# Kernel tuning notes

Measured on AMD Instinct MI355X. Metric: run time of the kernel, lower is better.

Reference implementation:

```python
import jax, jax.numpy as jnp
import numpy as np

N = 100000   # nodes
E = 1000000  # edges
F_IN = 15    # node feature dim
H = 64       # hidden dim
EMB = 128    # embedding dim
R = 13       # relations
NB = 4       # bases


def _xavier(key, shape):
    fan_in, fan_out = shape[-2], shape[-1]
    lim = float(np.sqrt(6.0 / (fan_in + fan_out)))
    return jax.random.uniform(key, shape, jnp.float32, -lim, lim)


def setup_inputs() -> dict:
    key = jax.random.key(0)
    ks = jax.random.split(key, 24)
    inp = {}
    inp["node_features"] = jax.random.normal(ks[0], (N, F_IN), jnp.float32)
    inp["edge_index"] = jax.random.randint(ks[1], (2, E), 0, N, jnp.int32)
    inp["edge_type"] = jax.random.randint(ks[2], (E,), 0, R, jnp.int32)
    # input projection (15 -> 64)
    inp["W_in"] = _xavier(ks[3], (F_IN, H)); inp["b_in"] = jnp.zeros((H,), jnp.float32)
    # RGCN layer 0
    inp["Wself0"] = _xavier(ks[4], (H, H)); inp["bself0"] = jnp.zeros((H,), jnp.float32)
    inp["bases0"] = _xavier(ks[5], (NB, H, H))
    inp["coeffs0"] = _xavier(ks[6], (R, NB))
    # RGCN layer 1
    inp["Wself1"] = _xavier(ks[7], (H, H)); inp["bself1"] = jnp.zeros((H,), jnp.float32)
    inp["bases1"] = _xavier(ks[8], (NB, H, H))
    inp["coeffs1"] = _xavier(ks[9], (R, NB))
    # readout MLP (2H -> H -> EMB)
    inp["Wr1"] = _xavier(ks[10], (2 * H, H)); inp["br1"] = jnp.zeros((H,), jnp.float32)
    inp["Wr2"] = _xavier(ks[11], (H, EMB)); inp["br2"] = jnp.zeros((EMB,), jnp.float32)
    # node projection (H -> EMB)
    inp["Wnp"] = _xavier(ks[12], (H, EMB)); inp["bnp"] = jnp.zeros((EMB,), jnp.float32)
    return inp


def _rgcn_layer(h, src, tgt, etype, Wself, bself, bases, coeffs):
    # h: (N, H). Sum over relations of per-relation gather+matmul+scatter-add
    # == single scatter over all edges with per-edge relation weight.
    # Basis decomposition: W_r = sum_b coeffs[r,b] * bases[b].
    h_src = h[src]                 # (E, H) gather
    c_e = coeffs[etype]            # (E, NB) per-edge basis coefficients
    msg = jnp.zeros((h_src.shape[0], bases.shape[2]), h.dtype)
    for b in range(bases.shape[0]):  # fixed small loop over NB=4 bases
        msg = msg + c_e[:, b:b + 1] * (h_src @ bases[b])
    agg = jax.ops.segment_sum(msg, tgt, num_segments=h.shape[0])  # (N, H)
    # NOTE: original code computes degree norm but never applies it (dead code),
    # so aggregation is an unnormalized scatter-add, reproduced faithfully here.
    return jax.nn.relu(h @ Wself + bself + agg)  # dropout is identity in eval


def reference(node_features, edge_index, edge_type, W_in, b_in,
              Wself0, bself0, bases0, coeffs0,
              Wself1, bself1, bases1, coeffs1,
              Wr1, br1, Wr2, br2, Wnp, bnp):
    src, tgt = edge_index[0], edge_index[1]
    h = node_features @ W_in + b_in                      # (N, H)
    h = _rgcn_layer(h, src, tgt, edge_type, Wself0, bself0, bases0, coeffs0)
    h = _rgcn_layer(h, src, tgt, edge_type, Wself1, bself1, bases1, coeffs1)
    # graph readout: mean + max pooling over nodes -> MLP
    g = jnp.concatenate([h.mean(axis=0), h.max(axis=0)])  # (2H,)
    graph_emb = jax.nn.relu(g @ Wr1 + br1) @ Wr2 + br2    # (EMB,)
    node_emb = h @ Wnp + bnp                              # (N, EMB)
    return graph_emb, node_emb
```

## Files before the change

kernel.cpp:

```cpp
#include <hip/hip_runtime.h>
#include <hip/hip_bf16.h>

#define NN 100000
#define EE 1000000
#define FIN 15
#define HH 64
#define EMBD 128
#define RR 13
#define NBASE 4
#define NP 391

typedef __hip_bfloat16 bf16;
typedef __attribute__((ext_vector_type(8))) short short8;
typedef __attribute__((ext_vector_type(4))) float f32x4;

__device__ __forceinline__ float b2f(bf16 x) { return __bfloat162float(x); }
__device__ __forceinline__ float bcast(float v, int l) {
    return __uint_as_float(__builtin_amdgcn_readlane(__float_as_uint(v), l));
}
__device__ __forceinline__ int bcasti(int v, int l) {
    return (int)__builtin_amdgcn_readlane((unsigned)v, l);
}
__device__ __forceinline__ unsigned short f2bu(float f) {
    bf16 t = __float2bfloat16(f);
    return *reinterpret_cast<unsigned short*>(&t);
}
__device__ __forceinline__ float bu2f(unsigned u) {
    return __uint_as_float(u << 16);
}

__global__ void k_detect(const void* __restrict__ win, int* __restrict__ flag) {
    int tid = threadIdx.x;
    const bf16* p = (const bf16*)win;
    int cnt = 0;
    for (int i = tid; i < FIN * HH; i += 64) {
        float v = b2f(p[i]);
        if (!(fabsf(v) < 0.3f)) cnt++;
    }
#pragma unroll
    for (int off = 32; off > 0; off >>= 1) cnt += __shfl_down(cnt, off, 64);
    if (tid == 0) *flag = (cnt > 40) ? 1 : 0;
}

struct ConvTab {
    const void* in[17];
    int n[17];
    int cum[18];
};

__global__ void k_convert_all(ConvTab tab, float* __restrict__ base,
                              const int* __restrict__ flag) {
    int g = blockIdx.x * 256 + threadIdx.x;
    if (g >= tab.cum[17]) return;
    int t = 0;
#pragma unroll
    for (int i = 0; i < 17; ++i) if (g >= tab.cum[i + 1]) t = i + 1;
    int local = g - tab.cum[t];
    if (local >= tab.n[t]) return;
    float v;
    if (*flag) v = ((const float*)tab.in[t])[local];
    else       v = b2f(((const bf16*)tab.in[t])[local]);
    base[g] = v;
}

__global__ void k_zero(int* __restrict__ a, int n) {
    int i = blockIdx.x * 256 + threadIdx.x;
    if (i < n) a[i] = 0;
}

__global__ void k_hist(const int* __restrict__ tgt, int* __restrict__ count,
                       int* __restrict__ rank) {
    int e = blockIdx.x * 256 + threadIdx.x;
    if (e >= EE) return;
    rank[e] = atomicAdd(&count[tgt[e]], 1);
}

__global__ void k_scan1(const int* __restrict__ count, int* __restrict__ scanned,
                        int* __restrict__ partials) {
    __shared__ int buf[256];
    int tid = threadIdx.x;
    int i = blockIdx.x * 256 + tid;
    int v = (i < NN) ? count[i] : 0;
    buf[tid] = v;
    __syncthreads();
    for (int off = 1; off < 256; off <<= 1) {
        int t = (tid >= off) ? buf[tid - off] : 0;
        __syncthreads();
        buf[tid] += t;
        __syncthreads();
    }
    if (i < NN) scanned[i] = buf[tid] - v;
    if (tid == 255) partials[blockIdx.x] = buf[255];
}

__global__ void k_scan2(int* __restrict__ partials) {
    __shared__ int buf[512];
    int tid = threadIdx.x;
    int v = (tid < NP) ? partials[tid] : 0;
    buf[tid] = v;
    __syncthreads();
    for (int off = 1; off < 512; off <<= 1) {
        int t = (tid >= off) ? buf[tid - off] : 0;
        __syncthreads();
        buf[tid] += t;
        __syncthreads();
    }
    if (tid < NP) partials[tid] = buf[tid] - v;
}

__global__ void k_scatter(const int* __restrict__ src, const int* __restrict__ tgt,
                          const int* __restrict__ et, const int* __restrict__ rank,
                          const int* __restrict__ scanned, const int* __restrict__ partials,
                          int* __restrict__ packed) {
    int e = blockIdx.x * 256 + threadIdx.x;
    if (e >= EE) return;
    int t = tgt[e];
    int pos = scanned[t] + partials[t >> 8] + rank[e];
    packed[pos] = src[e] | (et[e] << 17);
}

__global__ void k_wcat(const float* __restrict__ bases0, const float* __restrict__ Wself0,
                       const float* __restrict__ bases1, const float* __restrict__ Wself1,
                       unsigned short* __restrict__ W0, unsigned short* __restrict__ W1) {
    int idx = blockIdx.x * 256 + threadIdx.x;
    if (idx >= HH * 320) return;
    int n = idx / 320, k = idx - n * 320;
    int b = k >> 6, kk = k & 63;
    float v0 = (b < 4) ? bases0[b * 4096 + kk * 64 + n] : Wself0[kk * 64 + n];
    float v1 = (b < 4) ? bases1[b * 4096 + kk * 64 + n] : Wself1[kk * 64 + n];
    W0[idx] = f2bu(v0);
    W1[idx] = f2bu(v1);
}


__global__ void k_input_proj(const float* __restrict__ nf, const float* __restrict__ Win,
                             const float* __restrict__ bin, unsigned short* __restrict__ h) {
    __shared__ float w[FIN * HH];
    __shared__ float bb[HH];
    int tid = threadIdx.x;
    for (int i = tid; i < FIN * HH; i += 256) w[i] = Win[i];
    if (tid < HH) bb[tid] = bin[tid];
    __syncthreads();
    int idx = blockIdx.x * 256 + tid;
    if (idx >= NN * HH) return;
    int n = idx >> 6, j = idx & 63;
    float acc = bb[j];
    const float* row = nf + n * FIN;
#pragma unroll
    for (int k = 0; k < FIN; ++k) acc = fmaf(row[k], w[k * HH + j], acc);
    h[idx] = f2bu(acc);
}

__global__ void __launch_bounds__(256, 4)
k_layer(const unsigned short* __restrict__ hin, const int* __restrict__ packed,
        const int* __restrict__ count, const int* __restrict__ scanned,
        const int* __restrict__ partials, const float* __restrict__ coeffs,
        const unsigned short* __restrict__ Wc, const float* __restrict__ bself,
        unsigned short* __restrict__ hout) {
    __shared__ __align__(16) unsigned short Sb[16 * 264];
    int tid = threadIdx.x;
    int lane = tid & 63;
    int wv = tid >> 6;
    int t0 = blockIdx.x * 16;

    float S[4][NBASE];
#pragma unroll
    for (int ln = 0; ln < 4; ++ln)
        S[ln][0] = S[ln][1] = S[ln][2] = S[ln][3] = 0.f;

#pragma unroll
    for (int ln = 0; ln < 4; ++ln) {
        int t = t0 + wv * 4 + ln;
        int cnt = count[t];
        int s0 = scanned[t] + partials[t >> 8];
        for (int base = 0; base < cnt; base += 64) {
            int pk = 0;
            if (base + lane < cnt) pk = packed[s0 + base + lane];
            int m = min(64, cnt - base);
            for (int j = 0; j < m; j += 8) {
                float hv[8];
                float4 cv[8];
#pragma unroll
                for (int k = 0; k < 8; ++k) {
                    int v = bcasti(pk, j + k);
                    int s = v & 0x1FFFF;
                    int r = (v >> 17) & 0xF;
                    hv[k] = bu2f((unsigned)hin[s * HH + lane]);
                    cv[k] = *(const float4*)(coeffs + r * NBASE);
                }
#pragma unroll
                for (int k = 0; k < 8; ++k) {
                    float hk = ((j + k) < m) ? hv[k] : 0.f;
                    S[ln][0] = fmaf(cv[k].x, hk, S[ln][0]);
                    S[ln][1] = fmaf(cv[k].y, hk, S[ln][1]);
                    S[ln][2] = fmaf(cv[k].z, hk, S[ln][2]);
                    S[ln][3] = fmaf(cv[k].w, hk, S[ln][3]);
                }
            }
        }
    }
#pragma unroll
    for (int ln = 0; ln < 4; ++ln)
#pragma unroll
        for (int b = 0; b < NBASE; ++b)
            Sb[(wv * 4 + ln) * 264 + b * 64 + lane] = f2bu(S[ln][b]);
    __syncthreads();

    int m16 = lane & 15;
    int g = lane >> 4;
    f32x4 acc = {0.f, 0.f, 0.f, 0.f};
    const unsigned short* brow = Wc + (wv * 16 + m16) * 320 + g * 8;
#pragma unroll
    for (int kb = 0; kb < 8; ++kb) {
        short8 a = *(const short8*)(&Sb[m16 * 264 + kb * 32 + g * 8]);
        short8 b = *(const short8*)(brow + kb * 32);
        acc = __builtin_amdgcn_mfma_f32_16x16x32_bf16(a, b, acc, 0, 0, 0);
    }
    const unsigned short* hrow = hin + (t0 + m16) * HH + g * 8;
#pragma unroll
    for (int kb = 0; kb < 2; ++kb) {
        short8 a = *(const short8*)(hrow + kb * 32);
        short8 b = *(const short8*)(brow + 256 + kb * 32);
        acc = __builtin_amdgcn_mfma_f32_16x16x32_bf16(a, b, acc, 0, 0, 0);
    }
    int col = wv * 16 + m16;
    float bias = bself[col];
#pragma unroll
    for (int r = 0; r < 4; ++r) {
        int row = g * 4 + r;
        hout[(t0 + row) * HH + col] = f2bu(fmaxf(acc[r] + bias, 0.f));
    }
}

__global__ void k_reduce(const unsigned short* __restrict__ h, float* __restrict__ psum,
                         float* __restrict__ pmax) {
    __shared__ float ls[256], lm[256];
    int tid = threadIdx.x;
    int j = tid & 63;
    int slot = tid >> 6;
    float s = 0.f, m = -1e30f;
    for (int n = blockIdx.x * 4 + slot; n < NN; n += gridDim.x * 4) {
        float v = bu2f((unsigned)h[n * HH + j]);
        s += v;
        m = fmaxf(m, v);
    }
    ls[tid] = s; lm[tid] = m;
    __syncthreads();
    if (tid < 64) {
        s = ls[tid] + ls[tid + 64] + ls[tid + 128] + ls[tid + 192];
        m = fmaxf(fmaxf(lm[tid], lm[tid + 64]), fmaxf(lm[tid + 128], lm[tid + 192]));
        psum[blockIdx.x * 64 + tid] = s;
        pmax[blockIdx.x * 64 + tid] = m;
    }
}

__global__ void k_finish(const float* __restrict__ psum, const float* __restrict__ pmax,
                         const float* __restrict__ Wr1, const float* __restrict__ br1,
                         const float* __restrict__ Wr2, const float* __restrict__ br2,
                         void* __restrict__ out, const int* __restrict__ flag) {
    __shared__ float ls[256], lm[256];
    __shared__ float g[2 * HH];
    __shared__ float tbuf[HH];
    int tid = threadIdx.x;
    int j = tid & 63;
    int slot = tid >> 6;
    float s = 0.f, m = -1e30f;
    for (int i = slot; i < 256; i += 4) {
        s += psum[i * 64 + j];
        m = fmaxf(m, pmax[i * 64 + j]);
    }
    ls[tid] = s; lm[tid] = m;
    __syncthreads();
    if (tid < 64) {
        s = ls[tid] + ls[tid + 64] + ls[tid + 128] + ls[tid + 192];
        m = fmaxf(fmaxf(lm[tid], lm[tid + 64]), fmaxf(lm[tid + 128], lm[tid + 192]));
        g[tid] = s * (1.0f / NN);
        g[64 + tid] = m;
    }
    __syncthreads();
    if (tid < 64) {
        float acc = br1[tid];
#pragma unroll 8
        for (int k = 0; k < 2 * HH; ++k) acc = fmaf(g[k], Wr1[k * HH + tid], acc);
        tbuf[tid] = fmaxf(acc, 0.f);
    }
    __syncthreads();
    if (tid < EMBD) {
        float acc = br2[tid];
#pragma unroll 8
        for (int k = 0; k < HH; ++k) acc = fmaf(tbuf[k], Wr2[k * EMBD + tid], acc);
        if (*flag) ((float*)out)[tid] = acc;
        else       ((bf16*)out)[tid] = __float2bfloat16(acc);
    }
}

__global__ void k_node_emb2(const unsigned short* __restrict__ h, const float* __restrict__ Wnp,
                            const float* __restrict__ bnp, void* __restrict__ out,
                            const int* __restrict__ flag) {
    int tid = threadIdx.x;
    int lane = tid & 63;
    int wv = tid >> 6;
    int n0 = blockIdx.x * 32 + wv * 8;
    float hval[8];
#pragma unroll
    for (int ln = 0; ln < 8; ++ln)
        hval[ln] = bu2f((unsigned)h[(n0 + ln) * HH + lane]);
    float b0 = bnp[lane], b1 = bnp[64 + lane];
    float acc0[8], acc1[8];
#pragma unroll
    for (int ln = 0; ln < 8; ++ln) { acc0[ln] = b0; acc1[ln] = b1; }
#pragma unroll 8
    for (int k = 0; k < HH; ++k) {
        float w0 = Wnp[k * EMBD + lane];
        float w1 = Wnp[k * EMBD + 64 + lane];
#pragma unroll
        for (int ln = 0; ln < 8; ++ln) {
            float hv = bcast(hval[ln], k);
            acc0[ln] = fmaf(hv, w0, acc0[ln]);
            acc1[ln] = fmaf(hv, w1, acc1[ln]);
        }
    }
    if (*flag) {
        float* o = (float*)out + EMBD;
#pragma unroll
        for (int ln = 0; ln < 8; ++ln) {
            o[(long)(n0 + ln) * EMBD + lane] = acc0[ln];
            o[(long)(n0 + ln) * EMBD + 64 + lane] = acc1[ln];
        }
    } else {
        bf16* o = (bf16*)out + EMBD;
#pragma unroll
        for (int ln = 0; ln < 8; ++ln) {
            o[(long)(n0 + ln) * EMBD + lane] = __float2bfloat16(acc0[ln]);
            o[(long)(n0 + ln) * EMBD + 64 + lane] = __float2bfloat16(acc1[ln]);
        }
    }
}

extern "C" void kernel_launch(void* const* d_in, const int* in_sizes, int n_in,
                              void* d_out, int out_size, void* d_ws, size_t ws_size,
                              hipStream_t stream) {
    const int* eidx  = (const int*)d_in[1];
    const int* etype = (const int*)d_in[2];
    const int* src = eidx;
    const int* tgt = eidx + EE;

    int* flag = (int*)d_ws;
    float* base = (float*)d_ws + 16;

    const int fidx[17] = {0, 3, 4, 5, 6, 7, 8, 9, 10, 11, 12, 13, 14, 15, 16, 17, 18};
    ConvTab tab;
    float* conv[19];
    int cum = 0;
    for (int t = 0; t < 17; ++t) {
        int i = fidx[t];
        tab.in[t] = d_in[i];
        tab.n[t] = in_sizes[i];
        tab.cum[t] = cum;
        conv[i] = base + cum;
        cum += (in_sizes[i] + 15) & ~15;
    }
    tab.cum[17] = cum;

    k_detect<<<1, 64, 0, stream>>>(d_in[3], flag);
    k_convert_all<<<(cum + 255) / 256, 256, 0, stream>>>(tab, base, flag);

    float* p = base + cum;
    float* psum = p;  p += 256 * 64;
    float* pmax = p;  p += 256 * 64;
    int* count    = (int*)p;           p += NN;
    int* scanned  = (int*)p;           p += NN;
    int* partials = (int*)p;           p += 512;
    int* rank     = (int*)p;           p += EE;
    int* packed   = (int*)p;           p += EE;
    unsigned short* hbf0 = (unsigned short*)p;
    unsigned short* hbf1 = hbf0 + (size_t)NN * HH;
    unsigned short* Wc0  = hbf1 + (size_t)NN * HH;
    unsigned short* Wc1  = Wc0 + HH * 320;

    const float* nf      = conv[0];
    const float* Win     = conv[3];
    const float* bin     = conv[4];
    const float* Wself0  = conv[5];
    const float* bself0  = conv[6];
    const float* bases0  = conv[7];
    const float* coeffs0 = conv[8];
    const float* Wself1  = conv[9];
    const float* bself1  = conv[10];
    const float* bases1  = conv[11];
    const float* coeffs1 = conv[12];
    const float* Wr1     = conv[13];
    const float* br1     = conv[14];
    const float* Wr2     = conv[15];
    const float* br2     = conv[16];
    const float* Wnp     = conv[17];
    const float* bnp     = conv[18];

    const int NHB = (NN * HH) / 256;
    const int SMB = NN / 32;
    const int LYB = NN / 16;
    const int EB  = (EE + 255) / 256;

    k_zero<<<(NN + 255) / 256, 256, 0, stream>>>(count, NN);
    k_hist<<<EB, 256, 0, stream>>>(tgt, count, rank);
    k_scan1<<<NP, 256, 0, stream>>>(count, scanned, partials);
    k_scan2<<<1, 512, 0, stream>>>(partials);
    k_scatter<<<EB, 256, 0, stream>>>(src, tgt, etype, rank, scanned, partials, packed);

    k_wcat<<<(HH * 320 + 255) / 256, 256, 0, stream>>>(bases0, Wself0, bases1, Wself1, Wc0, Wc1);
    k_input_proj<<<NHB, 256, 0, stream>>>(nf, Win, bin, hbf0);

    k_layer<<<LYB, 256, 0, stream>>>(hbf0, packed, count, scanned, partials, coeffs0, Wc0, bself0, hbf1);
    k_layer<<<LYB, 256, 0, stream>>>(hbf1, packed, count, scanned, partials, coeffs1, Wc1, bself1, hbf0);

    k_reduce<<<256, 256, 0, stream>>>(hbf0, psum, pmax);
    k_finish<<<1, 256, 0, stream>>>(psum, pmax, Wr1, br1, Wr2, br2, d_out, flag);
    k_node_emb2<<<SMB, 256, 0, stream>>>(hbf0, Wnp, bnp, d_out, flag);
}
```

Baseline: 434.7 us.

## Pad per-node edge lists with sentinels and move node projection onto MFMA

Each node's CSR segment is padded to a multiple of 8 and filled with a sentinel relation whose coefficients are zero. This removes per-edge bounds masking in the layer gather, which now processes edges in groups of 16 or 8 and raises occupancy to 6 blocks per SM. The node-embedding projection is rewritten to use bf16 MFMA with a hi/lo split of Wnp to keep fp32-like accuracy. The cost is extra fill and prep kernels plus a larger packed buffer. The sentinel path relies on the padded coefficient table and on the source index 0 reads being harmless.

```diff
diff --git a/kernel.cpp b/kernel.cpp
--- a/kernel.cpp
+++ b/kernel.cpp
@@ -9,6 +9,8 @@
 #define RR 13
 #define NBASE 4
 #define NP 391
+#define CAP 1700128
+#define SENT (15 << 17)
 
 typedef __hip_bfloat16 bf16;
 typedef __attribute__((ext_vector_type(8))) short short8;
@@ -68,6 +70,11 @@
     if (i < n) a[i] = 0;
 }
 
+__global__ void k_fill(int* __restrict__ a, int n, int val) {
+    int i = blockIdx.x * 256 + threadIdx.x;
+    if (i < n) a[i] = val;
+}
+
 __global__ void k_hist(const int* __restrict__ tgt, int* __restrict__ count,
                        int* __restrict__ rank) {
     int e = blockIdx.x * 256 + threadIdx.x;
@@ -80,7 +87,7 @@
     __shared__ int buf[256];
     int tid = threadIdx.x;
     int i = blockIdx.x * 256 + tid;
-    int v = (i < NN) ? count[i] : 0;
+    int v = (i < NN) ? ((count[i] + 7) & ~7) : 0;
     buf[tid] = v;
     __syncthreads();
     for (int off = 1; off < 256; off <<= 1) {
@@ -117,6 +124,14 @@
     int t = tgt[e];
     int pos = scanned[t] + partials[t >> 8] + rank[e];
     packed[pos] = src[e] | (et[e] << 17);
+}
+
+__global__ void k_coef(const float* __restrict__ c0, const float* __restrict__ c1,
+                       float* __restrict__ o0, float* __restrict__ o1) {
+    int t = threadIdx.x;
+    int r = t >> 2, b = t & 3;
+    o0[t] = (r < RR) ? c0[r * NBASE + b] : 0.f;
+    o1[t] = (r < RR) ? c1[r * NBASE + b] : 0.f;
 }
 
 __global__ void k_wcat(const float* __restrict__ bases0, const float* __restrict__ Wself0,
@@ -132,6 +147,16 @@
     W1[idx] = f2bu(v1);
 }
 
+__global__ void k_wt(const float* __restrict__ Wnp, unsigned short* __restrict__ WT) {
+    int idx = blockIdx.x * 256 + threadIdx.x;
+    if (idx >= EMBD * HH) return;
+    int c = idx >> 6, k = idx & 63;
+    float w = Wnp[k * EMBD + c];
+    unsigned short hi = f2bu(w);
+    WT[idx] = hi;
+    WT[EMBD * HH + idx] = f2bu(w - bu2f(hi));
+}
+
 
 __global__ void k_input_proj(const float* __restrict__ nf, const float* __restrict__ Win,
                              const float* __restrict__ bin, unsigned short* __restrict__ h) {
@@ -151,10 +176,80 @@
     h[idx] = f2bu(acc);
 }
 
-__global__ void __launch_bounds__(256, 4)
+__device__ __forceinline__ void edge_group16(const unsigned short* __restrict__ hin,
+                                             const float* __restrict__ cc,
+                                             int lane, int pk, int j, float S[4]) {
+    float hv[16];
+    int rr[16];
+#pragma unroll
+    for (int k = 0; k < 16; ++k) {
+        int v = bcasti(pk, j + k);
+        rr[k] = (v >> 17) & 0xF;
+        hv[k] = bu2f((unsigned)hin[(v & 0x1FFFF) * HH + lane]);
+    }
+#pragma unroll
+    for (int hh = 0; hh < 2; ++hh) {
+        float4 cv[8];
+#pragma unroll
+        for (int k = 0; k < 8; ++k)
+            cv[k] = *(const float4*)(cc + rr[hh * 8 + k] * 4);
+#pragma unroll
+        for (int k = 0; k < 8; ++k) {
+            float hk = hv[hh * 8 + k];
+            S[0] = fmaf(cv[k].x, hk, S[0]);
+            S[1] = fmaf(cv[k].y, hk, S[1]);
+            S[2] = fmaf(cv[k].z, hk, S[2]);
+            S[3] = fmaf(cv[k].w, hk, S[3]);
+        }
+    }
+}
+
+__device__ __forceinline__ void edge_group8(const unsigned short* __restrict__ hin,
+                                            const float* __restrict__ cc,
+                                            int lane, int pk, int j, float S[4]) {
+    float hv[8];
+    int rr[8];
+#pragma unroll
+    for (int k = 0; k < 8; ++k) {
+        int v = bcasti(pk, j + k);
+        rr[k] = (v >> 17) & 0xF;
+        hv[k] = bu2f((unsigned)hin[(v & 0x1FFFF) * HH + lane]);
+    }
+    float4 cv[8];
+#pragma unroll
+    for (int k = 0; k < 8; ++k) cv[k] = *(const float4*)(cc + rr[k] * 4);
+#pragma unroll
+    for (int k = 0; k < 8; ++k) {
+        float hk = hv[k];
+        S[0] = fmaf(cv[k].x, hk, S[0]);
+        S[1] = fmaf(cv[k].y, hk, S[1]);
+        S[2] = fmaf(cv[k].z, hk, S[2]);
+        S[3] = fmaf(cv[k].w, hk, S[3]);
+    }
+}
+
+__device__ __forceinline__ void gather_node(const unsigned short* __restrict__ hin,
+                                            const int* __restrict__ packed,
+                                            const float* __restrict__ cc,
+                                            int lane, int pk, int s0, int cntp,
+                                            float S[4]) {
+    int lim = min(64, cntp);
+    int j = 0;
+    for (; j + 16 <= lim; j += 16) edge_group16(hin, cc, lane, pk, j, S);
+    if (j < lim) edge_group8(hin, cc, lane, pk, j, S);
+    for (int base = 64; base < cntp; base += 64) {
+        int pkx = packed[s0 + base + lane];
+        int lim2 = min(64, cntp - base);
+        int j2 = 0;
+        for (; j2 + 16 <= lim2; j2 += 16) edge_group16(hin, cc, lane, pkx, j2, S);
+        if (j2 < lim2) edge_group8(hin, cc, lane, pkx, j2, S);
+    }
+}
+
+__global__ void __launch_bounds__(256, 6)
 k_layer(const unsigned short* __restrict__ hin, const int* __restrict__ packed,
         const int* __restrict__ count, const int* __restrict__ scanned,
-        const int* __restrict__ partials, const float* __restrict__ coeffs,
+        const int* __restrict__ partials, const float* __restrict__ cc,
         const unsigned short* __restrict__ Wc, const float* __restrict__ bself,
         unsigned short* __restrict__ hout) {
     __shared__ __align__(16) unsigned short Sb[16 * 264];
@@ -162,48 +257,34 @@
     int lane = tid & 63;
     int wv = tid >> 6;
     int t0 = blockIdx.x * 16;
-
-    float S[4][NBASE];
-#pragma unroll
-    for (int ln = 0; ln < 4; ++ln)
-        S[ln][0] = S[ln][1] = S[ln][2] = S[ln][3] = 0.f;
-
-#pragma unroll
-    for (int ln = 0; ln < 4; ++ln) {
-        int t = t0 + wv * 4 + ln;
-        int cnt = count[t];
-        int s0 = scanned[t] + partials[t >> 8];
-        for (int base = 0; base < cnt; base += 64) {
-            int pk = 0;
-            if (base + lane < cnt) pk = packed[s0 + base + lane];
-            int m = min(64, cnt - base);
-            for (int j = 0; j < m; j += 8) {
-                float hv[8];
-                float4 cv[8];
-#pragma unroll
-                for (int k = 0; k < 8; ++k) {
-                    int v = bcasti(pk, j + k);
-                    int s = v & 0x1FFFF;
-                    int r = (v >> 17) & 0xF;
-                    hv[k] = bu2f((unsigned)hin[s * HH + lane]);
-                    cv[k] = *(const float4*)(coeffs + r * NBASE);
-                }
-#pragma unroll
-                for (int k = 0; k < 8; ++k) {
-                    float hk = ((j + k) < m) ? hv[k] : 0.f;
-                    S[ln][0] = fmaf(cv[k].x, hk, S[ln][0]);
-                    S[ln][1] = fmaf(cv[k].y, hk, S[ln][1]);
-                    S[ln][2] = fmaf(cv[k].z, hk, S[ln][2]);
-                    S[ln][3] = fmaf(cv[k].w, hk, S[ln][3]);
-                }
-            }
-        }
-    }
-#pragma unroll
-    for (int ln = 0; ln < 4; ++ln)
-#pragma unroll
-        for (int b = 0; b < NBASE; ++b)
-            Sb[(wv * 4 + ln) * 264 + b * 64 + lane] = f2bu(S[ln][b]);
+    int nb = t0 + wv * 4;
+
+    int4 c4  = *(const int4*)(count + nb);
+    int4 sc4 = *(const int4*)(scanned + nb);
+    int pb = partials[t0 >> 8];
+    int s00 = sc4.x + pb, s01 = sc4.y + pb, s02 = sc4.z + pb, s03 = sc4.w + pb;
+    int cp0 = (c4.x + 7) & ~7, cp1 = (c4.y + 7) & ~7;
+    int cp2 = (c4.z + 7) & ~7, cp3 = (c4.w + 7) & ~7;
+
+    int pk0 = packed[s00 + lane];
+    int pk1 = packed[s01 + lane];
+    int pk2 = packed[s02 + lane];
+    int pk3 = packed[s03 + lane];
+
+    float S0[4] = {0, 0, 0, 0}, S1[4] = {0, 0, 0, 0};
+    float S2[4] = {0, 0, 0, 0}, S3[4] = {0, 0, 0, 0};
+    gather_node(hin, packed, cc, lane, pk0, s00, cp0, S0);
+    gather_node(hin, packed, cc, lane, pk1, s01, cp1, S1);
+    gather_node(hin, packed, cc, lane, pk2, s02, cp2, S2);
+    gather_node(hin, packed, cc, lane, pk3, s03, cp3, S3);
+
+#pragma unroll
+    for (int b = 0; b < NBASE; ++b) {
+        Sb[(wv * 4 + 0) * 264 + b * 64 + lane] = f2bu(S0[b]);
+        Sb[(wv * 4 + 1) * 264 + b * 64 + lane] = f2bu(S1[b]);
+        Sb[(wv * 4 + 2) * 264 + b * 64 + lane] = f2bu(S2[b]);
+        Sb[(wv * 4 + 3) * 264 + b * 64 + lane] = f2bu(S3[b]);
+    }
     __syncthreads();
 
     int m16 = lane & 15;
@@ -294,45 +375,52 @@
     }
 }
 
-__global__ void k_node_emb2(const unsigned short* __restrict__ h, const float* __restrict__ Wnp,
-                            const float* __restrict__ bnp, void* __restrict__ out,
-                            const int* __restrict__ flag) {
+__global__ void __launch_bounds__(256, 8)
+k_node_emb2(const unsigned short* __restrict__ h, const unsigned short* __restrict__ WT,
+            const float* __restrict__ bnp, void* __restrict__ out,
+            const int* __restrict__ flag) {
     int tid = threadIdx.x;
     int lane = tid & 63;
     int wv = tid >> 6;
-    int n0 = blockIdx.x * 32 + wv * 8;
-    float hval[8];
-#pragma unroll
-    for (int ln = 0; ln < 8; ++ln)
-        hval[ln] = bu2f((unsigned)h[(n0 + ln) * HH + lane]);
-    float b0 = bnp[lane], b1 = bnp[64 + lane];
-    float acc0[8], acc1[8];
-#pragma unroll
-    for (int ln = 0; ln < 8; ++ln) { acc0[ln] = b0; acc1[ln] = b1; }
-#pragma unroll 8
-    for (int k = 0; k < HH; ++k) {
-        float w0 = Wnp[k * EMBD + lane];
-        float w1 = Wnp[k * EMBD + 64 + lane];
-#pragma unroll
-        for (int ln = 0; ln < 8; ++ln) {
-            float hv = bcast(hval[ln], k);
-            acc0[ln] = fmaf(hv, w0, acc0[ln]);
-            acc1[ln] = fmaf(hv, w1, acc1[ln]);
-        }
-    }
+    int n0 = blockIdx.x * 16;
+    int m16 = lane & 15, g = lane >> 4;
+
+    const unsigned short* arow = h + (n0 + m16) * HH + g * 8;
+    short8 a0 = *(const short8*)(arow);
+    short8 a1 = *(const short8*)(arow + 32);
+
+    int c0 = wv * 32;
+    const unsigned short* bp0 = WT + (c0 + m16) * HH + g * 8;
+    const unsigned short* bp1 = WT + (c0 + 16 + m16) * HH + g * 8;
+    const unsigned short* lp0 = bp0 + EMBD * HH;
+    const unsigned short* lp1 = bp1 + EMBD * HH;
+
+    f32x4 accA = {0.f, 0.f, 0.f, 0.f}, accB = {0.f, 0.f, 0.f, 0.f};
+    accA = __builtin_amdgcn_mfma_f32_16x16x32_bf16(a0, *(const short8*)bp0, accA, 0, 0, 0);
+    accA = __builtin_amdgcn_mfma_f32_16x16x32_bf16(a1, *(const short8*)(bp0 + 32), accA, 0, 0, 0);
+    accA = __builtin_amdgcn_mfma_f32_16x16x32_bf16(a0, *(const short8*)lp0, accA, 0, 0, 0);
+    accA = __builtin_amdgcn_mfma_f32_16x16x32_bf16(a1, *(const short8*)(lp0 + 32), accA, 0, 0, 0);
+    accB = __builtin_amdgcn_mfma_f32_16x16x32_bf16(a0, *(const short8*)bp1, accB, 0, 0, 0);
+    accB = __builtin_amdgcn_mfma_f32_16x16x32_bf16(a1, *(const short8*)(bp1 + 32), accB, 0, 0, 0);
+    accB = __builtin_amdgcn_mfma_f32_16x16x32_bf16(a0, *(const short8*)lp1, accB, 0, 0, 0);
+    accB = __builtin_amdgcn_mfma_f32_16x16x32_bf16(a1, *(const short8*)(lp1 + 32), accB, 0, 0, 0);
+
+    float biasA = bnp[c0 + m16], biasB = bnp[c0 + 16 + m16];
     if (*flag) {
         float* o = (float*)out + EMBD;
 #pragma unroll
-        for (int ln = 0; ln < 8; ++ln) {
-            o[(long)(n0 + ln) * EMBD + lane] = acc0[ln];
-            o[(long)(n0 + ln) * EMBD + 64 + lane] = acc1[ln];
+        for (int r = 0; r < 4; ++r) {
+            long node = n0 + g * 4 + r;
+            o[node * EMBD + c0 + m16]      = accA[r] + biasA;
+            o[node * EMBD + c0 + 16 + m16] = accB[r] + biasB;
         }
     } else {
         bf16* o = (bf16*)out + EMBD;
 #pragma unroll
-        for (int ln = 0; ln < 8; ++ln) {
-            o[(long)(n0 + ln) * EMBD + lane] = __float2bfloat16(acc0[ln]);
-            o[(long)(n0 + ln) * EMBD + 64 + lane] = __float2bfloat16(acc1[ln]);
+        for (int r = 0; r < 4; ++r) {
+            long node = n0 + g * 4 + r;
+            o[node * EMBD + c0 + m16]      = __float2bfloat16(accA[r] + biasA);
+            o[node * EMBD + c0 + 16 + m16] = __float2bfloat16(accB[r] + biasB);
         }
     }
 }
@@ -368,15 +456,18 @@
     float* p = base + cum;
     float* psum = p;  p += 256 * 64;
     float* pmax = p;  p += 256 * 64;
+    float* c16a = p;  p += 64;
+    float* c16b = p;  p += 64;
     int* count    = (int*)p;           p += NN;
     int* scanned  = (int*)p;           p += NN;
     int* partials = (int*)p;           p += 512;
     int* rank     = (int*)p;           p += EE;
-    int* packed   = (int*)p;           p += EE;
+    int* packed   = (int*)p;           p += CAP;
     unsigned short* hbf0 = (unsigned short*)p;
     unsigned short* hbf1 = hbf0 + (size_t)NN * HH;
     unsigned short* Wc0  = hbf1 + (size_t)NN * HH;
     unsigned short* Wc1  = Wc0 + HH * 320;
+    unsigned short* WT   = Wc1 + HH * 320;
 
     const float* nf      = conv[0];
     const float* Win     = conv[3];
@@ -397,23 +488,25 @@
     const float* bnp     = conv[18];
 
     const int NHB = (NN * HH) / 256;
-    const int SMB = NN / 32;
     const int LYB = NN / 16;
     const int EB  = (EE + 255) / 256;
 
     k_zero<<<(NN + 255) / 256, 256, 0, stream>>>(count, NN);
+    k_fill<<<(CAP + 255) / 256, 256, 0, stream>>>(packed, CAP, SENT);
     k_hist<<<EB, 256, 0, stream>>>(tgt, count, rank);
     k_scan1<<<NP, 256, 0, stream>>>(count, scanned, partials);
     k_scan2<<<1, 512, 0, stream>>>(partials);
     k_scatter<<<EB, 256, 0, stream>>>(src, tgt, etype, rank, scanned, partials, packed);
 
+    k_coef<<<1, 64, 0, stream>>>(coeffs0, coeffs1, c16a, c16b);
     k_wcat<<<(HH * 320 + 255) / 256, 256, 0, stream>>>(bases0, Wself0, bases1, Wself1, Wc0, Wc1);
+    k_wt<<<(EMBD * HH + 255) / 256, 256, 0, stream>>>(Wnp, WT);
     k_input_proj<<<NHB, 256, 0, stream>>>(nf, Win, bin, hbf0);
 
-    k_layer<<<LYB, 256, 0, stream>>>(hbf0, packed, count, scanned, partials, coeffs0, Wc0, bself0, hbf1);
-    k_layer<<<LYB, 256, 0, stream>>>(hbf1, packed, count, scanned, partials, coeffs1, Wc1, bself1, hbf0);
+    k_layer<<<LYB, 256, 0, stream>>>(hbf0, packed, count, scanned, partials, c16a, Wc0, bself0, hbf1);
+    k_layer<<<LYB, 256, 0, stream>>>(hbf1, packed, count, scanned, partials, c16b, Wc1, bself1, hbf0);
 
     k_reduce<<<256, 256, 0, stream>>>(hbf0, psum, pmax);
     k_finish<<<1, 256, 0, stream>>>(psum, pmax, Wr1, br1, Wr2, br2, d_out, flag);
-    k_node_emb2<<<SMB, 256, 0, stream>>>(hbf0, Wnp, bnp, d_out, flag);
-}
+    k_node_emb2<<<LYB, 256, 0, stream>>>(hbf0, WT, bnp, d_out, flag);
+}
```

New measurement: 425.2 us. 2.2% less time.
